# Kernel tuning notes

Hardware: AMD Instinct MI355X
Metric: run time of the kernel (lower is better)

Reference implementation:

```python
import jax, jax.numpy as jnp
import numpy as np

B, L, H, E, R = 4, 512, 768, 10, 10

def setup_inputs() -> dict:
    key = jax.random.key(0)
    ks = jax.random.split(key, 7)
    s = 1.0 / np.sqrt(H)
    return {
        "h": jax.random.normal(ks[0], (B, L, H), dtype=jnp.float32),
        "W_proj": jax.random.normal(ks[1], (H, H), dtype=jnp.float32) * s,
        "b_proj": jax.random.normal(ks[2], (H,), dtype=jnp.float32) * s,
        "W_ent": jax.random.normal(ks[3], (E, H), dtype=jnp.float32) * s,
        "b_ent": jax.random.normal(ks[4], (E,), dtype=jnp.float32) * s,
        "W_bil": jax.random.normal(ks[5], (R, H, H), dtype=jnp.float32) * s,
        "b_bil": jax.random.normal(ks[6], (R,), dtype=jnp.float32) * s,
    }

def reference(h, W_proj, b_proj, W_ent, b_ent, W_bil, b_bil):
    # h: (B, L, H)
    h_proj = jax.nn.relu(jnp.einsum('blh,kh->blk', h, W_proj) + b_proj)  # Linear: x @ W^T + b
    ent_logits = jnp.einsum('blh,eh->ble', h_proj, W_ent) + b_ent        # (B, L, E)
    # nn.Bilinear on all (i, j) pairs: rel[b,i,j,r] = h_i^T W_r h_j + b_r.
    # Factored O(L^2*H*R + L*H^2*R) instead of materializing (B,L,L,H) pairs.
    t = jnp.einsum('rhk,bmk->brmh', W_bil, h_proj)                        # (B, R, L, H)
    rel_logits = jnp.einsum('blh,brmh->blmr', h_proj, t) + b_bil          # (B, L, L, R)
    return (ent_logits, rel_logits)
```

## Files before the change

kernel.cpp:

```cpp
#include <hip/hip_runtime.h>
#include <stdint.h>

#define Bdim 4
#define Ldim 512
#define Hdim 768
#define Edim 10
#define Rdim 10

typedef __attribute__((ext_vector_type(8))) short short8;
typedef __attribute__((ext_vector_type(4))) float floatx4;

__device__ __forceinline__ unsigned short f2bf(float x) {
    unsigned int u = __float_as_uint(x);
    unsigned int r = (u + 0x7fffu + ((u >> 16) & 1u)) >> 16;
    return (unsigned short)r;
}
__device__ __forceinline__ float bf2f(unsigned short u) {
    return __uint_as_float(((unsigned int)u) << 16);
}

#define GLOAD_LDS16(g, l)                                                      \
    __builtin_amdgcn_global_load_lds(                                          \
        (const __attribute__((address_space(1))) void*)(g),                    \
        (__attribute__((address_space(3))) void*)(l), 16, 0, 0)

__global__ void k_cvt4(const float* __restrict__ s0, unsigned short* __restrict__ d0, int n0,
                       const float* __restrict__ s1, unsigned short* __restrict__ d1, int n1,
                       const float* __restrict__ s2, unsigned short* __restrict__ d2, int n2,
                       const float* __restrict__ s3, unsigned short* __restrict__ d3, int n3) {
    int total = n0 + n1 + n2 + n3;
    int i = blockIdx.x * blockDim.x + threadIdx.x;
    int stride = gridDim.x * blockDim.x;
    for (; i < total; i += stride) {
        const float* s; unsigned short* d; int j = i;
        if (j < n0) { s = s0; d = d0; }
        else { j -= n0;
            if (j < n1) { s = s1; d = d1; }
            else { j -= n1;
                if (j < n2) { s = s2; d = d2; }
                else { j -= n2; s = s3; d = d3; }
            }
        }
        float4 v = reinterpret_cast<const float4*>(s)[j];
        ushort4 o;
        o.x = f2bf(v.x); o.y = f2bf(v.y); o.z = f2bf(v.z); o.w = f2bf(v.w);
        reinterpret_cast<ushort4*>(d)[j] = o;
    }
}

__device__ __forceinline__ int xcd_swz(int bid, int nwg) {
    int cpx = nwg >> 3;
    return (bid & 7) * cpx + (bid >> 3);
}

__device__ __forceinline__ void gemm_bt_core64_db(
    const unsigned short* __restrict__ A, int lda,
    const unsigned short* __restrict__ Bm, int ldb,
    int K,
    unsigned short* lA, unsigned short* lB,
    floatx4 acc[4][4])
{
    const int tid  = threadIdx.x;
    const int lane = tid & 63;
    const int wave = tid >> 6;
    const int wr = wave >> 1;
    const int wc = wave & 1;

    const int srow   = tid >> 3;
    const int schunk = (tid & 7) ^ (srow & 7);
    const int skk    = schunk << 3;

    const int frow = lane & 15;
    const int fs   = lane >> 4;

    #pragma unroll
    for (int i = 0; i < 4; ++i) {
        GLOAD_LDS16(A  + (size_t)(srow + 32 * i) * lda + skk,
                    lA + (tid + 256 * i) * 8);
        GLOAD_LDS16(Bm + (size_t)(srow + 32 * i) * ldb + skk,
                    lB + (tid + 256 * i) * 8);
    }
    __syncthreads();

    const int nt = K >> 6;
    int buf = 0;
    for (int kt = 0; kt < nt; ++kt) {
        if (kt + 1 < nt) {
            const int k0n = (kt + 1) << 6;
            unsigned short* dA = lA + (buf ^ 1) * 8192;
            unsigned short* dB = lB + (buf ^ 1) * 8192;
            #pragma unroll
            for (int i = 0; i < 4; ++i) {
                GLOAD_LDS16(A  + (size_t)(srow + 32 * i) * lda + k0n + skk,
                            dA + (tid + 256 * i) * 8);
                GLOAD_LDS16(Bm + (size_t)(srow + 32 * i) * ldb + k0n + skk,
                            dB + (tid + 256 * i) * 8);
            }
        }
        const unsigned short* sA = lA + buf * 8192;
        const unsigned short* sB = lB + buf * 8192;
        #pragma unroll
        for (int h = 0; h < 2; ++h) {
            short8 af[4], bfr[4];
            #pragma unroll
            for (int mi = 0; mi < 4; ++mi) {
                int row  = wr * 64 + mi * 16 + frow;
                int slot = (fs + 4 * h) ^ (row & 7);
                af[mi] = *reinterpret_cast<const short8*>(sA + row * 64 + slot * 8);
            }
            #pragma unroll
            for (int ni = 0; ni < 4; ++ni) {
                int row  = wc * 64 + ni * 16 + frow;
                int slot = (fs + 4 * h) ^ (row & 7);
                bfr[ni] = *reinterpret_cast<const short8*>(sB + row * 64 + slot * 8);
            }
            #pragma unroll
            for (int mi = 0; mi < 4; ++mi)
                #pragma unroll
                for (int ni = 0; ni < 4; ++ni)
                    acc[mi][ni] = __builtin_amdgcn_mfma_f32_16x16x32_bf16(
                        af[mi], bfr[ni], acc[mi][ni], 0, 0, 0);
        }
        __syncthreads();
        buf ^= 1;
    }
}

__device__ __forceinline__ void gemm_bt_core256_db(
    const unsigned short* __restrict__ A, int lda,
    const unsigned short* __restrict__ Bm, int ldb,
    int K,
    unsigned short* lA, unsigned short* lB,
    floatx4 acc[8][4])
{
    const int tid  = threadIdx.x;
    const int lane = tid & 63;
    const int wave = tid >> 6;
    const int wr = wave >> 2;
    const int wc = wave & 3;

    const int srow   = tid >> 3;
    const int schunk = (tid & 7) ^ (srow & 7);
    const int skk    = schunk << 3;

    const int frow = lane & 15;
    const int fs   = lane >> 4;

    #pragma unroll
    for (int i = 0; i < 4; ++i) {
        GLOAD_LDS16(A  + (size_t)(srow + 64 * i) * lda + skk,
                    lA + (tid + 512 * i) * 8);
        GLOAD_LDS16(Bm + (size_t)(srow + 64 * i) * ldb + skk,
                    lB + (tid + 512 * i) * 8);
    }
    __syncthreads();

    const int nt = K >> 6;
    int buf = 0;
    for (int kt = 0; kt < nt; ++kt) {
        if (kt + 1 < nt) {
            const int k0n = (kt + 1) << 6;
            unsigned short* dA = lA + (buf ^ 1) * 16384;
            unsigned short* dB = lB + (buf ^ 1) * 16384;
            #pragma unroll
            for (int i = 0; i < 4; ++i) {
                GLOAD_LDS16(A  + (size_t)(srow + 64 * i) * lda + k0n + skk,
                            dA + (tid + 512 * i) * 8);
                GLOAD_LDS16(Bm + (size_t)(srow + 64 * i) * ldb + k0n + skk,
                            dB + (tid + 512 * i) * 8);
            }
        }
        const unsigned short* sA = lA + buf * 16384;
        const unsigned short* sB = lB + buf * 16384;
        #pragma unroll
        for (int h = 0; h < 2; ++h) {
            short8 bfr[4];
            #pragma unroll
            for (int ni = 0; ni < 4; ++ni) {
                int row  = wc * 64 + ni * 16 + frow;
                int slot = (fs + 4 * h) ^ (row & 7);
                bfr[ni] = *reinterpret_cast<const short8*>(sB + row * 64 + slot * 8);
            }
            #pragma unroll
            for (int mi = 0; mi < 8; ++mi) {
                int row  = wr * 128 + mi * 16 + frow;
                int slot = (fs + 4 * h) ^ (row & 7);
                short8 af = *reinterpret_cast<const short8*>(sA + row * 64 + slot * 8);
                #pragma unroll
                for (int ni = 0; ni < 4; ++ni)
                    acc[mi][ni] = __builtin_amdgcn_mfma_f32_16x16x32_bf16(
                        af, bfr[ni], acc[mi][ni], 0, 0, 0);
            }
        }
        __syncthreads();
        buf ^= 1;
    }
}

__global__ __launch_bounds__(256) void k_gemm_proj(
    const unsigned short* __restrict__ hA,
    const unsigned short* __restrict__ Wp,
    const float* __restrict__ bproj,
    unsigned short* __restrict__ hp)
{
    __shared__ unsigned short lA[2 * 128 * 64];
    __shared__ unsigned short lB[2 * 128 * 64];
    int bid = xcd_swz(blockIdx.x + gridDim.x * blockIdx.y, gridDim.x * gridDim.y);
    const int m0 = (bid % gridDim.x) * 128;
    const int n0 = (bid / gridDim.x) * 128;
    floatx4 acc[4][4];
    #pragma unroll
    for (int i = 0; i < 4; ++i)
        #pragma unroll
        for (int j = 0; j < 4; ++j)
            acc[i][j] = (floatx4){0.f, 0.f, 0.f, 0.f};

    gemm_bt_core64_db(hA + (size_t)m0 * Hdim, Hdim,
                      Wp + (size_t)n0 * Hdim, Hdim, Hdim, lA, lB, acc);

    const int tid = threadIdx.x, lane = tid & 63, wave = tid >> 6;
    const int wr = wave >> 1, wc = wave & 1;
    const int cl = lane & 15, rh = (lane >> 4) * 4;
    #pragma unroll
    for (int mi = 0; mi < 4; ++mi)
        #pragma unroll
        for (int ni = 0; ni < 4; ++ni)
            #pragma unroll
            for (int j = 0; j < 4; ++j) {
                int r = m0 + wr * 64 + mi * 16 + rh + j;
                int c = n0 + wc * 64 + ni * 16 + cl;
                float v = acc[mi][ni][j] + bproj[c];
                hp[(size_t)r * Hdim + c] = f2bf(fmaxf(v, 0.0f));
            }
}

__global__ __launch_bounds__(512, 1) void k_gemm_t(
    const unsigned short* __restrict__ hp,
    const unsigned short* __restrict__ Wb,
    unsigned short* __restrict__ T)
{
    __shared__ unsigned short lA[2 * 256 * 64];
    __shared__ unsigned short lB[2 * 256 * 64];
    int bid = xcd_swz(blockIdx.x + gridDim.x * blockIdx.y, gridDim.x * gridDim.y);
    const int m0 = (bid % gridDim.x) * 256;
    const int n0 = (bid / gridDim.x) * 256;
    floatx4 acc[8][4];
    #pragma unroll
    for (int i = 0; i < 8; ++i)
        #pragma unroll
        for (int j = 0; j < 4; ++j)
            acc[i][j] = (floatx4){0.f, 0.f, 0.f, 0.f};

    gemm_bt_core256_db(hp + (size_t)m0 * Hdim, Hdim,
                       Wb + (size_t)n0 * Hdim, Hdim, Hdim, lA, lB, acc);

    const int tid = threadIdx.x, lane = tid & 63, wave = tid >> 6;
    const int wr = wave >> 2, wc = wave & 3;
    const int cl = lane & 15, rh = (lane >> 4) * 4;
    #pragma unroll
    for (int mi = 0; mi < 8; ++mi)
        #pragma unroll
        for (int ni = 0; ni < 4; ++ni)
            #pragma unroll
            for (int j = 0; j < 4; ++j) {
                int r = m0 + wr * 128 + mi * 16 + rh + j;
                int c = n0 + wc * 64 + ni * 16 + cl;
                T[(size_t)r * (Rdim * Hdim) + c] = f2bf(acc[mi][ni][j]);
            }
}

__global__ __launch_bounds__(512, 1) void k_gemm_rel(
    const unsigned short* __restrict__ hp,
    const unsigned short* __restrict__ T,
    const float* __restrict__ bbil,
    float* __restrict__ rel)
{
    __shared__ unsigned short lA[2 * 256 * 64];
    __shared__ unsigned short lB[2 * 256 * 64];
    int bid = xcd_swz(blockIdx.x + gridDim.x * blockIdx.y, gridDim.x * gridDim.y);
    const int m0 = (bid % gridDim.x) * 256;
    const int n0 = (bid / gridDim.x) * 256;
    const int b  = m0 >> 9;
    floatx4 acc[8][4];
    #pragma unroll
    for (int i = 0; i < 8; ++i)
        #pragma unroll
        for (int j = 0; j < 4; ++j)
            acc[i][j] = (floatx4){0.f, 0.f, 0.f, 0.f};

    const unsigned short* Ab = hp + (size_t)m0 * Hdim;
    const unsigned short* Bb = T + (size_t)b * Ldim * (Rdim * Hdim) + (size_t)n0 * Hdim;
    gemm_bt_core256_db(Ab, Hdim, Bb, Hdim, Hdim, lA, lB, acc);

    const int tid = threadIdx.x, lane = tid & 63, wave = tid >> 6;
    const int wr = wave >> 2, wc = wave & 3;
    const int cl = lane & 15, rh = (lane >> 4) * 4;
    #pragma unroll
    for (int mi = 0; mi < 8; ++mi)
        #pragma unroll
        for (int ni = 0; ni < 4; ++ni) {
            int n = n0 + wc * 64 + ni * 16 + cl;
            float bias = bbil[n % Rdim];
            #pragma unroll
            for (int j = 0; j < 4; ++j) {
                int grow = m0 + wr * 128 + mi * 16 + rh + j;
                rel[(size_t)grow * (Ldim * Rdim) + n] = acc[mi][ni][j] + bias;
            }
        }
}

__global__ __launch_bounds__(256) void k_ent(
    const unsigned short* __restrict__ hp,
    const unsigned short* __restrict__ We,
    const float* __restrict__ bent,
    float* __restrict__ out)
{
    const int gw = (blockIdx.x * blockDim.x + threadIdx.x) >> 6;
    const int lane = threadIdx.x & 63;
    if (gw >= Bdim * Ldim) return;
    const unsigned short* row = hp + (size_t)gw * Hdim;
    float hv[12];
    #pragma unroll
    for (int j = 0; j < 12; ++j) hv[j] = bf2f(row[lane + j * 64]);
    #pragma unroll
    for (int e = 0; e < Edim; ++e) {
        const unsigned short* wrow = We + e * Hdim;
        float s = 0.f;
        #pragma unroll
        for (int j = 0; j < 12; ++j) s += hv[j] * bf2f(wrow[lane + j * 64]);
        #pragma unroll
        for (int off = 32; off >= 1; off >>= 1) s += __shfl_xor(s, off);
        if (lane == 0) out[(size_t)gw * Edim + e] = s + bent[e];
    }
}

extern "C" void kernel_launch(void* const* d_in, const int* in_sizes, int n_in,
                              void* d_out, int out_size, void* d_ws, size_t ws_size,
                              hipStream_t stream)
{
    const float* h     = (const float*)d_in[0];
    const float* Wproj = (const float*)d_in[1];
    const float* bproj = (const float*)d_in[2];
    const float* Went  = (const float*)d_in[3];
    const float* bent  = (const float*)d_in[4];
    const float* Wbil  = (const float*)d_in[5];
    const float* bbil  = (const float*)d_in[6];

    float* out_ent = (float*)d_out;
    float* out_rel = (float*)d_out + (size_t)Bdim * Ldim * Edim;

    unsigned short* h_bf  = (unsigned short*)d_ws;
    unsigned short* Wp_bf = h_bf  + (size_t)2048 * Hdim;
    unsigned short* Wb_bf = Wp_bf + (size_t)Hdim * Hdim;
    unsigned short* We_bf = Wb_bf + (size_t)Rdim * Hdim * Hdim;
    unsigned short* hp_bf = We_bf + (size_t)Edim * Hdim;
    unsigned short* T_bf  = hp_bf + (size_t)2048 * Hdim;

    {
        int n0 = 2048 * Hdim / 4;
        int n1 = Hdim * Hdim / 4;
        int n2 = Rdim * Hdim * Hdim / 4;
        int n3 = Edim * Hdim / 4;
        k_cvt4<<<dim3(2048), 256, 0, stream>>>(h, h_bf, n0, Wproj, Wp_bf, n1,
                                               Wbil, Wb_bf, n2, Went, We_bf, n3);
    }

    k_gemm_proj<<<dim3(2048 / 128, Hdim / 128), 256, 0, stream>>>(h_bf, Wp_bf, bproj, hp_bf);

    k_ent<<<dim3((Bdim * Ldim * 64) / 256), 256, 0, stream>>>(hp_bf, We_bf, bent, out_ent);

    k_gemm_t<<<dim3(2048 / 256, (Rdim * Hdim) / 256), 512, 0, stream>>>(hp_bf, Wb_bf, T_bf);

    k_gemm_rel<<<dim3(2048 / 256, (Ldim * Rdim) / 256), 512, 0, stream>>>(hp_bf, T_bf, bbil, out_rel);
}
```

Before: 174.5 us.

## Replace double-buffered GEMM core with four-stage K32 pipeline using vmcnt waits

The 256x256 GEMM core used by the T and rel kernels moves from a two-buffer K=64 loop to a four-stage ring of K=32 slices. Three slices are prefetched, and each step waits with a partial s_waitcnt vmcnt and a single barrier instead of a full __syncthreads per tile. LDS offsets are precomputed and use a new 4-chunk XOR swizzle. This keeps more global loads in flight to hide memory latency and removes barriers, but it hardcodes K=768 and depends on the compiler keeping the issue order the manual waitcnt counts assume.

After: 188.5 us. 1.08x slower.

```diff
diff --git a/kernel.cpp b/kernel.cpp
--- a/kernel.cpp
+++ b/kernel.cpp
@@ -23,6 +23,8 @@
     __builtin_amdgcn_global_load_lds(                                          \
         (const __attribute__((address_space(1))) void*)(g),                    \
         (__attribute__((address_space(3))) void*)(l), 16, 0, 0)
+
+#define WAITVM(n) asm volatile("s_waitcnt vmcnt(" #n ")" ::: "memory")
 
 __global__ void k_cvt4(const float* __restrict__ s0, unsigned short* __restrict__ d0, int n0,
                        const float* __restrict__ s1, unsigned short* __restrict__ d1, int n1,
@@ -126,10 +128,9 @@
     }
 }
 
-__device__ __forceinline__ void gemm_bt_core256_db(
+__device__ __forceinline__ void gemm_bt_core256_p4(
     const unsigned short* __restrict__ A, int lda,
     const unsigned short* __restrict__ Bm, int ldb,
-    int K,
     unsigned short* lA, unsigned short* lB,
     floatx4 acc[8][4])
 {
@@ -139,62 +140,81 @@
     const int wr = wave >> 2;
     const int wc = wave & 3;
 
-    const int srow   = tid >> 3;
-    const int schunk = (tid & 7) ^ (srow & 7);
-    const int skk    = schunk << 3;
+    const int srow0 = tid >> 2;
+    const int pchk  = tid & 3;
+    const int swz0  = ((srow0 ^ (srow0 >> 2)) & 3);
+    const int lchk  = pchk ^ swz0;
+    const unsigned short* pA0 = A  + (size_t)srow0 * lda + lchk * 8;
+    const unsigned short* pA1 = A  + (size_t)(srow0 + 128) * lda + lchk * 8;
+    const unsigned short* pB0 = Bm + (size_t)srow0 * ldb + lchk * 8;
+    const unsigned short* pB1 = Bm + (size_t)(srow0 + 128) * ldb + lchk * 8;
 
     const int frow = lane & 15;
     const int fs   = lane >> 4;
-
-    #pragma unroll
-    for (int i = 0; i < 4; ++i) {
-        GLOAD_LDS16(A  + (size_t)(srow + 64 * i) * lda + skk,
-                    lA + (tid + 512 * i) * 8);
-        GLOAD_LDS16(Bm + (size_t)(srow + 64 * i) * ldb + skk,
-                    lB + (tid + 512 * i) * 8);
-    }
-    __syncthreads();
-
-    const int nt = K >> 6;
-    int buf = 0;
-    for (int kt = 0; kt < nt; ++kt) {
-        if (kt + 1 < nt) {
-            const int k0n = (kt + 1) << 6;
-            unsigned short* dA = lA + (buf ^ 1) * 16384;
-            unsigned short* dB = lB + (buf ^ 1) * 16384;
-            #pragma unroll
-            for (int i = 0; i < 4; ++i) {
-                GLOAD_LDS16(A  + (size_t)(srow + 64 * i) * lda + k0n + skk,
-                            dA + (tid + 512 * i) * 8);
-                GLOAD_LDS16(Bm + (size_t)(srow + 64 * i) * ldb + k0n + skk,
-                            dB + (tid + 512 * i) * 8);
-            }
-        }
-        const unsigned short* sA = lA + buf * 16384;
-        const unsigned short* sB = lB + buf * 16384;
-        #pragma unroll
-        for (int h = 0; h < 2; ++h) {
-            short8 bfr[4];
-            #pragma unroll
-            for (int ni = 0; ni < 4; ++ni) {
-                int row  = wc * 64 + ni * 16 + frow;
-                int slot = (fs + 4 * h) ^ (row & 7);
-                bfr[ni] = *reinterpret_cast<const short8*>(sB + row * 64 + slot * 8);
-            }
-            #pragma unroll
-            for (int mi = 0; mi < 8; ++mi) {
-                int row  = wr * 128 + mi * 16 + frow;
-                int slot = (fs + 4 * h) ^ (row & 7);
-                short8 af = *reinterpret_cast<const short8*>(sA + row * 64 + slot * 8);
-                #pragma unroll
-                for (int ni = 0; ni < 4; ++ni)
-                    acc[mi][ni] = __builtin_amdgcn_mfma_f32_16x16x32_bf16(
-                        af, bfr[ni], acc[mi][ni], 0, 0, 0);
-            }
-        }
-        __syncthreads();
-        buf ^= 1;
-    }
+    int offA[8], offB[4];
+    #pragma unroll
+    for (int mi = 0; mi < 8; ++mi) {
+        int row  = wr * 128 + mi * 16 + frow;
+        int slot = fs ^ ((row ^ (row >> 2)) & 3);
+        offA[mi] = row * 32 + slot * 8;
+    }
+    #pragma unroll
+    for (int ni = 0; ni < 4; ++ni) {
+        int row  = wc * 64 + ni * 16 + frow;
+        int slot = fs ^ ((row ^ (row >> 2)) & 3);
+        offB[ni] = row * 32 + slot * 8;
+    }
+
+    #define STAGE_P4(s)                                                        \
+        do {                                                                   \
+            GLOAD_LDS16(pA0, lA + (s) * 8192 + tid * 8);                       \
+            GLOAD_LDS16(pA1, lA + (s) * 8192 + (tid + 512) * 8);               \
+            GLOAD_LDS16(pB0, lB + (s) * 8192 + tid * 8);                       \
+            GLOAD_LDS16(pB1, lB + (s) * 8192 + (tid + 512) * 8);               \
+            pA0 += 32; pA1 += 32; pB0 += 32; pB1 += 32;                        \
+        } while (0)
+
+    #define COMPUTE_P4(s)                                                      \
+        do {                                                                   \
+            const unsigned short* sA = lA + (s) * 8192;                        \
+            const unsigned short* sB = lB + (s) * 8192;                        \
+            short8 af[8], bfr[4];                                              \
+            _Pragma("unroll")                                                  \
+            for (int ni = 0; ni < 4; ++ni)                                     \
+                bfr[ni] = *reinterpret_cast<const short8*>(sB + offB[ni]);     \
+            _Pragma("unroll")                                                  \
+            for (int mi = 0; mi < 8; ++mi)                                     \
+                af[mi] = *reinterpret_cast<const short8*>(sA + offA[mi]);      \
+            _Pragma("unroll")                                                  \
+            for (int mi = 0; mi < 8; ++mi)                                     \
+                _Pragma("unroll")                                              \
+                for (int ni = 0; ni < 4; ++ni)                                 \
+                    acc[mi][ni] = __builtin_amdgcn_mfma_f32_16x16x32_bf16(     \
+                        af[mi], bfr[ni], acc[mi][ni], 0, 0, 0);                \
+        } while (0)
+
+    STAGE_P4(0);
+    STAGE_P4(1);
+    STAGE_P4(2);
+
+    for (int k = 0; k < 22; ++k) {
+        WAITVM(8);
+        __builtin_amdgcn_s_barrier();
+        if (k < 21) {
+            const int s = (k + 3) & 3;
+            STAGE_P4(s);
+        }
+        COMPUTE_P4(k & 3);
+    }
+    WAITVM(4);
+    __builtin_amdgcn_s_barrier();
+    COMPUTE_P4(22 & 3);
+    WAITVM(0);
+    __builtin_amdgcn_s_barrier();
+    COMPUTE_P4(23 & 3);
+
+    #undef STAGE_P4
+    #undef COMPUTE_P4
 }
 
 __global__ __launch_bounds__(256) void k_gemm_proj(
@@ -239,8 +259,8 @@
     const unsigned short* __restrict__ Wb,
     unsigned short* __restrict__ T)
 {
-    __shared__ unsigned short lA[2 * 256 * 64];
-    __shared__ unsigned short lB[2 * 256 * 64];
+    __shared__ unsigned short lA[4 * 256 * 32];
+    __shared__ unsigned short lB[4 * 256 * 32];
     int bid = xcd_swz(blockIdx.x + gridDim.x * blockIdx.y, gridDim.x * gridDim.y);
     const int m0 = (bid % gridDim.x) * 256;
     const int n0 = (bid / gridDim.x) * 256;
@@ -251,8 +271,8 @@
         for (int j = 0; j < 4; ++j)
             acc[i][j] = (floatx4){0.f, 0.f, 0.f, 0.f};
 
-    gemm_bt_core256_db(hp + (size_t)m0 * Hdim, Hdim,
-                       Wb + (size_t)n0 * Hdim, Hdim, Hdim, lA, lB, acc);
+    gemm_bt_core256_p4(hp + (size_t)m0 * Hdim, Hdim,
+                       Wb + (size_t)n0 * Hdim, Hdim, lA, lB, acc);
 
     const int tid = threadIdx.x, lane = tid & 63, wave = tid >> 6;
     const int wr = wave >> 2, wc = wave & 3;
@@ -275,8 +295,8 @@
     const float* __restrict__ bbil,
     float* __restrict__ rel)
 {
-    __shared__ unsigned short lA[2 * 256 * 64];
-    __shared__ unsigned short lB[2 * 256 * 64];
+    __shared__ unsigned short lA[4 * 256 * 32];
+    __shared__ unsigned short lB[4 * 256 * 32];
     int bid = xcd_swz(blockIdx.x + gridDim.x * blockIdx.y, gridDim.x * gridDim.y);
     const int m0 = (bid % gridDim.x) * 256;
     const int n0 = (bid / gridDim.x) * 256;
@@ -290,7 +310,7 @@
 
     const unsigned short* Ab = hp + (size_t)m0 * Hdim;
     const unsigned short* Bb = T + (size_t)b * Ldim * (Rdim * Hdim) + (size_t)n0 * Hdim;
-    gemm_bt_core256_db(Ab, Hdim, Bb, Hdim, Hdim, lA, lB, acc);
+    gemm_bt_core256_p4(Ab, Hdim, Bb, Hdim, lA, lB, acc);
 
     const int tid = threadIdx.x, lane = tid & 63, wave = tid >> 6;
     const int wr = wave >> 2, wc = wave & 3;
```
